# Kernel tuning notes

Hardware: AMD Instinct MI355X
Metric: run time of the kernel (lower is better)

The kernel has to match this reference:

```python
import jax, jax.numpy as jnp
import numpy as np

N, E, F, H, C, L = 50000, 800000, 32, 4, 32, 3
HC = H * C
NEG = 0.2  # leaky_relu negative slope (GATv2Conv default and explicit LeakyReLU(0.2))


def _gat_layer(x, src, dst, ea, Wl, bl, Wr, br, att, We, cb, lW, lb, bsc, bsh):
    # GATv2 linear transforms: [N, F] -> [N, H, C]
    xl = (x @ Wl + bl).reshape(N, H, C)
    xr = (x @ Wr + br).reshape(N, H, C)
    xj = xl[src]            # [E, H, C] messages from source nodes
    xi = xr[dst]            # [E, H, C] target-side features
    ep = (ea[:, None] @ We).reshape(E, H, C)  # edge-linear, edge_dim=1
    e = jax.nn.leaky_relu(xi + xj + ep, NEG)
    logits = jnp.einsum('ehc,hc->eh', e, att)            # [E, H]
    # segment softmax over destination node neighborhoods
    m = jax.ops.segment_max(logits, dst, num_segments=N)
    a = jnp.exp(logits - m[dst])
    denom = jax.ops.segment_sum(a, dst, num_segments=N)
    alpha = a / denom[dst]                               # [E, H]
    msg = xj * alpha[..., None]                          # [E, H, C]
    out = jax.ops.segment_sum(msg, dst, num_segments=N).reshape(N, HC) + cb
    # trailing per-layer MLP: Linear -> LeakyReLU(0.2) -> BatchNorm1d (eval, affine)
    h = jax.nn.leaky_relu(out @ lW + lb, NEG)
    return h * bsc + bsh


def setup_inputs() -> dict:
    key = jax.random.key(0)
    ks = jax.random.split(key, 24)
    s = 0.1
    inp = {
        'x': jax.random.normal(ks[0], (N, F), jnp.float32),
        'edge_index': jax.random.randint(ks[1], (2, E), 0, N, jnp.int32),
        'edge_attr': jax.random.normal(ks[2], (E,), jnp.float32),
        'batch': jnp.zeros((N,), jnp.int32),
        # stacked per-layer conv params (all 3 layers share shapes: F==hidden)
        'Wl': jax.random.normal(ks[3], (L, F, HC), jnp.float32) * s,
        'bl': jnp.zeros((L, HC), jnp.float32),
        'Wr': jax.random.normal(ks[4], (L, F, HC), jnp.float32) * s,
        'br': jnp.zeros((L, HC), jnp.float32),
        'att': jax.random.normal(ks[5], (L, H, C), jnp.float32) * s,
        'We': jax.random.normal(ks[6], (L, 1, HC), jnp.float32) * s,
        'conv_b': jnp.zeros((L, HC), jnp.float32),
        'lin_W': jax.random.normal(ks[7], (L, HC, F), jnp.float32) * s,
        'lin_b': jnp.zeros((L, F), jnp.float32),
        'bn_scale': jnp.ones((L, F), jnp.float32),
        'bn_shift': jnp.zeros((L, F), jnp.float32),
        # fcn head: hidden -> 256 -> 32 -> num_classes
        'W1': jax.random.normal(ks[8], (F, 256), jnp.float32) * s,
        'b1': jnp.zeros((256,), jnp.float32),
        'W2': jax.random.normal(ks[9], (256, 32), jnp.float32) * s,
        'b2': jnp.zeros((32,), jnp.float32),
        'W3': jax.random.normal(ks[10], (32, 2), jnp.float32) * s,
        'b3': jnp.zeros((2,), jnp.float32),
    }
    return inp


def reference(x, edge_index, edge_attr, batch, Wl, bl, Wr, br, att, We, conv_b,
              lin_W, lin_b, bn_scale, bn_shift, W1, b1, W2, b2, W3, b3):
    src, dst = edge_index[0], edge_index[1]
    ea = jnp.abs(edge_attr)
    h = x
    for i in range(L):
        h = _gat_layer(h, src, dst, ea, Wl[i], bl[i], Wr[i], br[i], att[i],
                       We[i], conv_b[i], lin_W[i], lin_b[i], bn_scale[i], bn_shift[i])
    # global mean pool over graphs in batch (single graph here, B=1)
    B = 1
    sums = jax.ops.segment_sum(h, batch, num_segments=B)
    cnts = jax.ops.segment_sum(jnp.ones((N, 1), h.dtype), batch, num_segments=B)
    g = sums / cnts
    g = jax.nn.leaky_relu(g @ W1 + b1, NEG)
    g = jax.nn.leaky_relu(g @ W2 + b2, NEG)
    return g @ W3 + b3
```

## Files before the change

kernel.cpp:

```cpp
#include <hip/hip_runtime.h>
#include <hip/hip_bf16.h>
#include <math.h>

#define NN 50000
#define EE 800000
#define HC 128
#define FF 32
#define NEG 0.2f


__global__ void k_hist(const int* __restrict__ dst, int* __restrict__ deg) {
    int e = blockIdx.x * 256 + threadIdx.x;
    if (e < EE) atomicAdd(&deg[dst[e]], 1);
}

__global__ void k_scan1(const int* __restrict__ deg, int* __restrict__ part) {
    __shared__ int sd[256];
    int b = blockIdx.x, t = threadIdx.x;
    int base = b * 1024 + t * 4;
    int s = 0;
#pragma unroll
    for (int i = 0; i < 4; ++i) { int idx = base + i; if (idx < NN) s += deg[idx]; }
    sd[t] = s; __syncthreads();
    for (int off = 128; off; off >>= 1) { if (t < off) sd[t] += sd[t + off]; __syncthreads(); }
    if (t == 0) part[b] = sd[0];
}

__global__ void k_scan2(int* __restrict__ part, int nb) {
    if (threadIdx.x == 0) {
        int run = 0;
        for (int i = 0; i < nb; ++i) { int v = part[i]; part[i] = run; run += v; }
    }
}

__global__ void k_scan3(const int* __restrict__ deg, const int* __restrict__ part,
                        int* __restrict__ rowptr) {
    __shared__ int sd[256];
    int b = blockIdx.x, t = threadIdx.x;
    int base = b * 1024 + t * 4;
    int v[4]; int mine = 0;
#pragma unroll
    for (int i = 0; i < 4; ++i) { int idx = base + i; v[i] = (idx < NN) ? deg[idx] : 0; mine += v[i]; }
    sd[t] = mine; __syncthreads();
    for (int off = 1; off < 256; off <<= 1) {
        int tmp = (t >= off) ? sd[t - off] : 0;
        __syncthreads();
        sd[t] += tmp;
        __syncthreads();
    }
    int run = sd[t] - mine + part[b];
#pragma unroll
    for (int i = 0; i < 4; ++i) { int idx = base + i; if (idx < NN) rowptr[idx] = run; run += v[i]; }
    if (b == 0 && t == 0) rowptr[NN] = EE;
}

__global__ void k_scatter(const int* __restrict__ src, const int* __restrict__ dst,
                          const float* __restrict__ ea, const int* __restrict__ rowptr,
                          int* __restrict__ fill, int2* __restrict__ pairs) {
    int e = blockIdx.x * 256 + threadIdx.x;
    if (e >= EE) return;
    int d = dst[e];
    int pos = rowptr[d] + atomicAdd(&fill[d], 1);
    pairs[pos] = make_int2(src[e], __float_as_int(fabsf(ea[e])));
}


__global__ __launch_bounds__(256) void k_dual_linear(
        const float* __restrict__ x,
        const float* __restrict__ Wl, const float* __restrict__ bl,
        const float* __restrict__ Wr, const float* __restrict__ br,
        float* __restrict__ xl, float* __restrict__ xr) {
    const int t = threadIdx.x;
    const int l = t & 63;
    const int half = l >> 5;
    const int lc = l & 31;
    const float* __restrict__ W  = half ? Wr : Wl;
    const float* __restrict__ bb = half ? br : bl;
    float* __restrict__ outp     = half ? xr : xl;

    float4 w[32];
#pragma unroll
    for (int k = 0; k < 32; ++k)
        w[k] = *(const float4*)(W + k * 128 + 4 * lc);
    const float4 bias = *(const float4*)(bb + 4 * lc);

    const int gw = blockIdx.x * 4 + (t >> 6);
    const int nW = gridDim.x * 4;
    const int q8 = 4 * (l & 7);

    int n = gw;
    if (n >= NN) return;
    float4 r0 = *(const float4*)(x + (size_t)n * 32 + q8);
    int n1 = n + nW < NN ? n + nW : n;
    float4 r1 = *(const float4*)(x + (size_t)n1 * 32 + q8);

    for (; n < NN; n += nW) {
        float4 cur = r0;
        r0 = r1;
        int np = n + 2 * nW < NN ? n + 2 * nW : n;
        r1 = *(const float4*)(x + (size_t)np * 32 + q8);

        float4 acc = bias;
#pragma unroll
        for (int q = 0; q < 8; ++q) {
            float vx = __shfl(cur.x, q, 8);
            float vy = __shfl(cur.y, q, 8);
            float vz = __shfl(cur.z, q, 8);
            float vw = __shfl(cur.w, q, 8);
            acc.x = fmaf(vx, w[4 * q + 0].x, acc.x);
            acc.y = fmaf(vx, w[4 * q + 0].y, acc.y);
            acc.z = fmaf(vx, w[4 * q + 0].z, acc.z);
            acc.w = fmaf(vx, w[4 * q + 0].w, acc.w);
            acc.x = fmaf(vy, w[4 * q + 1].x, acc.x);
            acc.y = fmaf(vy, w[4 * q + 1].y, acc.y);
            acc.z = fmaf(vy, w[4 * q + 1].z, acc.z);
            acc.w = fmaf(vy, w[4 * q + 1].w, acc.w);
            acc.x = fmaf(vz, w[4 * q + 2].x, acc.x);
            acc.y = fmaf(vz, w[4 * q + 2].y, acc.y);
            acc.z = fmaf(vz, w[4 * q + 2].z, acc.z);
            acc.w = fmaf(vz, w[4 * q + 2].w, acc.w);
            acc.x = fmaf(vw, w[4 * q + 3].x, acc.x);
            acc.y = fmaf(vw, w[4 * q + 3].y, acc.y);
            acc.z = fmaf(vw, w[4 * q + 3].z, acc.z);
            acc.w = fmaf(vw, w[4 * q + 3].w, acc.w);
        }
        *(float4*)(outp + (size_t)n * 128 + 4 * lc) = acc;
    }
}


__global__ __launch_bounds__(256) void k_gat_agg(
        const float* __restrict__ xl, const float* __restrict__ xr,
        const int* __restrict__ rowptr, const int2* __restrict__ pairs,
        const float* __restrict__ att,
        const float* __restrict__ Wev,
        const float* __restrict__ cb,
        float* __restrict__ outb) {
    const int l = threadIdx.x & 31;
    const int n = blockIdx.x * 8 + (threadIdx.x >> 5);
    const float4* __restrict__ xl4 = (const float4*)xl;

    float4 att4 = ((const float4*)att)[l];
    float4 we4  = ((const float4*)Wev)[l];
    float4 xr4  = ((const float4*)xr)[n * 32 + l];
    const int beg = rowptr[n], end = rowptr[n + 1];

    float m = -INFINITY, s = 0.f;
    float4 acc = make_float4(0.f, 0.f, 0.f, 0.f);

    int2 p0 = make_int2(0, 0), p1 = p0, p2 = p0, p3 = p0;
    float4 x0 = make_float4(0.f, 0.f, 0.f, 0.f), x1 = x0;
    if (beg     < end) p0 = pairs[beg];
    if (beg + 1 < end) p1 = pairs[beg + 1];
    if (beg + 2 < end) p2 = pairs[beg + 2];
    if (beg + 3 < end) p3 = pairs[beg + 3];
    if (beg     < end) x0 = xl4[(size_t)p0.x * 32 + l];
    if (beg + 1 < end) x1 = xl4[(size_t)p1.x * 32 + l];

#pragma unroll 2
    for (int j = beg; j < end; ++j) {
        int2 pn = p0; float4 xn = x0;
        if (j + 4 < end) pn = pairs[j + 4];
        if (j + 2 < end) xn = xl4[(size_t)p2.x * 32 + l];

        float sea = __int_as_float(p0.y);
        float4 v;
        v.x = fmaf(sea, we4.x, xr4.x + x0.x);
        v.y = fmaf(sea, we4.y, xr4.y + x0.y);
        v.z = fmaf(sea, we4.z, xr4.z + x0.z);
        v.w = fmaf(sea, we4.w, xr4.w + x0.w);
        v.x = fmaxf(v.x, NEG * v.x);
        v.y = fmaxf(v.y, NEG * v.y);
        v.z = fmaxf(v.z, NEG * v.z);
        v.w = fmaxf(v.w, NEG * v.w);
        float pl = v.x * att4.x;
        pl = fmaf(v.y, att4.y, pl);
        pl = fmaf(v.z, att4.z, pl);
        pl = fmaf(v.w, att4.w, pl);
        pl += __shfl_xor(pl, 4);
        pl += __shfl_xor(pl, 2);
        pl += __shfl_xor(pl, 1);

        if (pl <= m) {
            float e = __expf(pl - m);
            s += e;
            acc.x = fmaf(e, x0.x, acc.x);
            acc.y = fmaf(e, x0.y, acc.y);
            acc.z = fmaf(e, x0.z, acc.z);
            acc.w = fmaf(e, x0.w, acc.w);
        } else {
            float c = __expf(m - pl);
            s = fmaf(s, c, 1.f);
            acc.x = fmaf(acc.x, c, x0.x);
            acc.y = fmaf(acc.y, c, x0.y);
            acc.z = fmaf(acc.z, c, x0.z);
            acc.w = fmaf(acc.w, c, x0.w);
            m = pl;
        }
        p0 = p1; p1 = p2; p2 = p3; p3 = pn;
        x0 = x1; x1 = xn;
    }

    float inv = (s > 0.f) ? 1.f / s : 0.f;
    float4 cb4 = ((const float4*)cb)[l];
    float4 o;
    o.x = fmaf(acc.x, inv, cb4.x);
    o.y = fmaf(acc.y, inv, cb4.y);
    o.z = fmaf(acc.z, inv, cb4.z);
    o.w = fmaf(acc.w, inv, cb4.w);
    ((float4*)outb)[n * 32 + l] = o;
}


__global__ __launch_bounds__(256) void k_mlp_bn(
        const float* __restrict__ outb,
        const float* __restrict__ lW, const float* __restrict__ lb,
        const float* __restrict__ bsc, const float* __restrict__ bsh,
        float* __restrict__ h) {
    const int t = threadIdx.x;
    const int l = t & 63;
    const int half = l >> 5;
    const int cg = (l >> 2) & 7;
    const int kg = l & 3;

    float4 w[32];
#pragma unroll
    for (int kl = 0; kl < 32; ++kl)
        w[kl] = *(const float4*)(lW + (size_t)(32 * kg + kl) * 32 + 4 * cg);

    const float4 bias = (kg == 0) ? *(const float4*)(lb + 4 * cg)
                                  : make_float4(0.f, 0.f, 0.f, 0.f);
    const float4 sc4 = *(const float4*)(bsc + 4 * cg);
    const float4 sh4 = *(const float4*)(bsh + 4 * cg);

    const int gw = blockIdx.x * 4 + (t >> 6);
    const int nW = gridDim.x * 4;
    const int quad = 4 * (l & 31);
    const int kg8 = kg * 8;

    int p = gw;
    if (p >= NN / 2) return;
    float4 r0 = *(const float4*)(outb + (size_t)(2 * p + half) * 128 + quad);
    int p1i = p + nW < NN / 2 ? p + nW : p;
    float4 r1 = *(const float4*)(outb + (size_t)(2 * p1i + half) * 128 + quad);

    for (; p < NN / 2; p += nW) {
        float4 cur = r0;
        r0 = r1;
        int pp = p + 2 * nW < NN / 2 ? p + 2 * nW : p;
        r1 = *(const float4*)(outb + (size_t)(2 * pp + half) * 128 + quad);

        float4 acc = bias;
#pragma unroll
        for (int j = 0; j < 8; ++j) {
            float vx = __shfl(cur.x, kg8 + j, 32);
            float vy = __shfl(cur.y, kg8 + j, 32);
            float vz = __shfl(cur.z, kg8 + j, 32);
            float vw = __shfl(cur.w, kg8 + j, 32);
            acc.x = fmaf(vx, w[4 * j + 0].x, acc.x);
            acc.y = fmaf(vx, w[4 * j + 0].y, acc.y);
            acc.z = fmaf(vx, w[4 * j + 0].z, acc.z);
            acc.w = fmaf(vx, w[4 * j + 0].w, acc.w);
            acc.x = fmaf(vy, w[4 * j + 1].x, acc.x);
            acc.y = fmaf(vy, w[4 * j + 1].y, acc.y);
            acc.z = fmaf(vy, w[4 * j + 1].z, acc.z);
            acc.w = fmaf(vy, w[4 * j + 1].w, acc.w);
            acc.x = fmaf(vz, w[4 * j + 2].x, acc.x);
            acc.y = fmaf(vz, w[4 * j + 2].y, acc.y);
            acc.z = fmaf(vz, w[4 * j + 2].z, acc.z);
            acc.w = fmaf(vz, w[4 * j + 2].w, acc.w);
            acc.x = fmaf(vw, w[4 * j + 3].x, acc.x);
            acc.y = fmaf(vw, w[4 * j + 3].y, acc.y);
            acc.z = fmaf(vw, w[4 * j + 3].z, acc.z);
            acc.w = fmaf(vw, w[4 * j + 3].w, acc.w);
        }
        acc.x += __shfl_xor(acc.x, 1); acc.x += __shfl_xor(acc.x, 2);
        acc.y += __shfl_xor(acc.y, 1); acc.y += __shfl_xor(acc.y, 2);
        acc.z += __shfl_xor(acc.z, 1); acc.z += __shfl_xor(acc.z, 2);
        acc.w += __shfl_xor(acc.w, 1); acc.w += __shfl_xor(acc.w, 2);

        if (kg == 0) {
            float4 o;
            o.x = fmaxf(acc.x, NEG * acc.x);
            o.y = fmaxf(acc.y, NEG * acc.y);
            o.z = fmaxf(acc.z, NEG * acc.z);
            o.w = fmaxf(acc.w, NEG * acc.w);
            o.x = fmaf(o.x, sc4.x, sh4.x);
            o.y = fmaf(o.y, sc4.y, sh4.y);
            o.z = fmaf(o.z, sc4.z, sh4.z);
            o.w = fmaf(o.w, sc4.w, sh4.w);
            *(float4*)(h + (size_t)(2 * p + half) * 32 + 4 * cg) = o;
        }
    }
}


__global__ void k_colsum(const float* __restrict__ h, float* __restrict__ g) {
    __shared__ float sd[256];
    int t = threadIdx.x;
    int col = t & 31, r = t >> 5;
    float local = 0.f;
    for (int row = blockIdx.x * 8 + r; row < NN; row += gridDim.x * 8)
        local += h[row * FF + col];
    sd[t] = local; __syncthreads();
    if (r < 4) sd[t] += sd[t + 128];
    __syncthreads();
    if (r < 2) sd[t] += sd[t + 64];
    __syncthreads();
    if (r < 1) atomicAdd(&g[col], sd[t] + sd[t + 32]);
}


__global__ void k_head(const float* __restrict__ g,
                       const float* __restrict__ W1, const float* __restrict__ b1,
                       const float* __restrict__ W2, const float* __restrict__ b2,
                       const float* __restrict__ W3, const float* __restrict__ b3,
                       float* __restrict__ out) {
    __shared__ float gv[32];
    __shared__ float h1[256];
    __shared__ float h2[32];
    int t = threadIdx.x;
    if (t < 32) gv[t] = g[t] * (1.0f / NN);
    __syncthreads();
    float acc = b1[t];
#pragma unroll 8
    for (int k = 0; k < 32; ++k) acc += gv[k] * W1[k * 256 + t];
    h1[t] = acc > 0.f ? acc : NEG * acc;
    __syncthreads();
    if (t < 32) {
        float a = b2[t];
        for (int k = 0; k < 256; ++k) a += h1[k] * W2[k * 32 + t];
        h2[t] = a > 0.f ? a : NEG * a;
    }
    __syncthreads();
    if (t < 2) {
        float a = b3[t];
#pragma unroll
        for (int k = 0; k < 32; ++k) a += h2[k] * W3[k * 2 + t];
        out[t] = a;
    }
}


static inline size_t alignup(size_t x) { return (x + 255) & ~size_t(255); }

extern "C" void kernel_launch(void* const* d_in, const int* in_sizes, int n_in,
                              void* d_out, int out_size, void* d_ws, size_t ws_size,
                              hipStream_t stream) {
    const float* x     = (const float*)d_in[0];
    const int*   eidx  = (const int*)d_in[1];
    const float* eattr = (const float*)d_in[2];
    const float* Wl    = (const float*)d_in[4];
    const float* bl    = (const float*)d_in[5];
    const float* Wr    = (const float*)d_in[6];
    const float* br    = (const float*)d_in[7];
    const float* att   = (const float*)d_in[8];
    const float* We    = (const float*)d_in[9];
    const float* cb    = (const float*)d_in[10];
    const float* lW    = (const float*)d_in[11];
    const float* lb    = (const float*)d_in[12];
    const float* bsc   = (const float*)d_in[13];
    const float* bsh   = (const float*)d_in[14];
    const float* W1    = (const float*)d_in[15];
    const float* b1    = (const float*)d_in[16];
    const float* W2    = (const float*)d_in[17];
    const float* b2    = (const float*)d_in[18];
    const float* W3    = (const float*)d_in[19];
    const float* b3    = (const float*)d_in[20];

    const int* srcp = eidx;
    const int* dstp = eidx + EE;

    char* ws = (char*)d_ws;
    size_t off = 0;
    float* xl     = (float*)(ws + off); off += alignup((size_t)NN * HC * 4);
    float* xr     = (float*)(ws + off); off += alignup((size_t)NN * HC * 4);
    float* outb   = (float*)(ws + off); off += alignup((size_t)NN * HC * 4);
    float* hA     = (float*)(ws + off); off += alignup((size_t)NN * FF * 4);
    float* hB     = (float*)(ws + off); off += alignup((size_t)NN * FF * 4);
    int2*  pairs  = (int2*) (ws + off); off += alignup((size_t)EE * 8);
    int*   rowptr = (int*)  (ws + off); off += alignup((size_t)(NN + 1) * 4);
    int*   deg    = (int*)  (ws + off); off += alignup((size_t)NN * 4);
    int*   fill   = (int*)  (ws + off); off += alignup((size_t)NN * 4);
    int*   part   = (int*)  (ws + off); off += alignup(64 * 4);
    float* g      = (float*)(ws + off); off += alignup(32 * 4);

    hipMemsetAsync(deg, 0, (size_t)NN * 4, stream);
    hipMemsetAsync(fill, 0, (size_t)NN * 4, stream);
    hipMemsetAsync(g, 0, 32 * 4, stream);

    const int nChunk = (NN + 1023) / 1024;
    k_hist<<<(EE + 255) / 256, 256, 0, stream>>>(dstp, deg);
    k_scan1<<<nChunk, 256, 0, stream>>>(deg, part);
    k_scan2<<<1, 64, 0, stream>>>(part, nChunk);
    k_scan3<<<nChunk, 256, 0, stream>>>(deg, part, rowptr);
    k_scatter<<<(EE + 255) / 256, 256, 0, stream>>>(srcp, dstp, eattr, rowptr, fill, pairs);

    const float* cur = x;
    float* hbuf[2] = {hA, hB};
    for (int i = 0; i < 3; ++i) {
        k_dual_linear<<<768, 256, 0, stream>>>(cur, Wl + i * FF * HC, bl + i * HC,
                                               Wr + i * FF * HC, br + i * HC, xl, xr);
        k_gat_agg<<<NN / 8, 256, 0, stream>>>(xl, xr, rowptr, pairs,
                                              att + i * HC, We + i * HC, cb + i * HC, outb);
        k_mlp_bn<<<768, 256, 0, stream>>>(outb, lW + i * HC * FF, lb + i * FF,
                                          bsc + i * FF, bsh + i * FF, hbuf[i & 1]);
        cur = hbuf[i & 1];
    }

    k_colsum<<<128, 256, 0, stream>>>(cur, g);
    k_head<<<1, 256, 0, stream>>>(g, W1, b1, W2, b2, W3, b3, (float*)d_out);
}
```

Baseline: 555.2 us.

## Merge scan kernels, make online softmax branchless, drop memsets and colsum atomics

Replaces the three-kernel prefix scan with a single-block scan, which cuts launch count but serialises about 200 elements per thread in one block. The GAT aggregation loop becomes branchless: each edge computes two exps with a running max instead of a divergent branch. Prefetch indices are clamped rather than guarded, and addresses are computed with byte shifts. The colsum atomics are replaced by per-block partials that the head kernel reduces. The deg and fill memsets are merged into one and the g memset is dropped.

```diff
diff --git a/kernel.cpp b/kernel.cpp
--- a/kernel.cpp
+++ b/kernel.cpp
@@ -14,44 +14,28 @@
     if (e < EE) atomicAdd(&deg[dst[e]], 1);
 }
 
-__global__ void k_scan1(const int* __restrict__ deg, int* __restrict__ part) {
-    __shared__ int sd[256];
-    int b = blockIdx.x, t = threadIdx.x;
-    int base = b * 1024 + t * 4;
+__global__ __launch_bounds__(256) void k_scan(const int* __restrict__ deg,
+                                              int* __restrict__ rowptr) {
+    __shared__ int sums[256];
+    const int t = threadIdx.x;
+    const int CH = (NN + 255) >> 8;
+    const int b0 = t * CH;
+    const int b1 = b0 + CH < NN ? b0 + CH : NN;
     int s = 0;
-#pragma unroll
-    for (int i = 0; i < 4; ++i) { int idx = base + i; if (idx < NN) s += deg[idx]; }
-    sd[t] = s; __syncthreads();
-    for (int off = 128; off; off >>= 1) { if (t < off) sd[t] += sd[t + off]; __syncthreads(); }
-    if (t == 0) part[b] = sd[0];
-}
-
-__global__ void k_scan2(int* __restrict__ part, int nb) {
-    if (threadIdx.x == 0) {
-        int run = 0;
-        for (int i = 0; i < nb; ++i) { int v = part[i]; part[i] = run; run += v; }
-    }
-}
-
-__global__ void k_scan3(const int* __restrict__ deg, const int* __restrict__ part,
-                        int* __restrict__ rowptr) {
-    __shared__ int sd[256];
-    int b = blockIdx.x, t = threadIdx.x;
-    int base = b * 1024 + t * 4;
-    int v[4]; int mine = 0;
-#pragma unroll
-    for (int i = 0; i < 4; ++i) { int idx = base + i; v[i] = (idx < NN) ? deg[idx] : 0; mine += v[i]; }
-    sd[t] = mine; __syncthreads();
+    for (int i = b0; i < b1; ++i) s += deg[i];
+    sums[t] = s;
+    __syncthreads();
+    int acc = s;
     for (int off = 1; off < 256; off <<= 1) {
-        int tmp = (t >= off) ? sd[t - off] : 0;
+        int tmp = (t >= off) ? sums[t - off] : 0;
         __syncthreads();
-        sd[t] += tmp;
+        acc += tmp;
+        sums[t] = acc;
         __syncthreads();
     }
-    int run = sd[t] - mine + part[b];
-#pragma unroll
-    for (int i = 0; i < 4; ++i) { int idx = base + i; if (idx < NN) rowptr[idx] = run; run += v[i]; }
-    if (b == 0 && t == 0) rowptr[NN] = EE;
+    int run = acc - s;
+    for (int i = b0; i < b1; ++i) { rowptr[i] = run; run += deg[i]; }
+    if (t == 255) rowptr[NN] = EE;
 }
 
 __global__ void k_scatter(const int* __restrict__ src, const int* __restrict__ dst,
@@ -138,67 +122,61 @@
         float* __restrict__ outb) {
     const int l = threadIdx.x & 31;
     const int n = blockIdx.x * 8 + (threadIdx.x >> 5);
-    const float4* __restrict__ xl4 = (const float4*)xl;
+    const char* __restrict__ xlp = (const char*)xl + (l << 4);
 
     float4 att4 = ((const float4*)att)[l];
     float4 we4  = ((const float4*)Wev)[l];
     float4 xr4  = ((const float4*)xr)[n * 32 + l];
     const int beg = rowptr[n], end = rowptr[n + 1];
+    const int last = end - 1;
 
     float m = -INFINITY, s = 0.f;
     float4 acc = make_float4(0.f, 0.f, 0.f, 0.f);
 
-    int2 p0 = make_int2(0, 0), p1 = p0, p2 = p0, p3 = p0;
-    float4 x0 = make_float4(0.f, 0.f, 0.f, 0.f), x1 = x0;
-    if (beg     < end) p0 = pairs[beg];
-    if (beg + 1 < end) p1 = pairs[beg + 1];
-    if (beg + 2 < end) p2 = pairs[beg + 2];
-    if (beg + 3 < end) p3 = pairs[beg + 3];
-    if (beg     < end) x0 = xl4[(size_t)p0.x * 32 + l];
-    if (beg + 1 < end) x1 = xl4[(size_t)p1.x * 32 + l];
+    if (beg < end) {
+        int2 p0 = pairs[beg];
+        int2 p1 = pairs[beg + 1 < last ? beg + 1 : last];
+        int2 p2 = pairs[beg + 2 < last ? beg + 2 : last];
+        float4 x0 = *(const float4*)(xlp + (p0.x << 9));
+        float4 x1 = *(const float4*)(xlp + (p1.x << 9));
 
 #pragma unroll 2
-    for (int j = beg; j < end; ++j) {
-        int2 pn = p0; float4 xn = x0;
-        if (j + 4 < end) pn = pairs[j + 4];
-        if (j + 2 < end) xn = xl4[(size_t)p2.x * 32 + l];
-
-        float sea = __int_as_float(p0.y);
-        float4 v;
-        v.x = fmaf(sea, we4.x, xr4.x + x0.x);
-        v.y = fmaf(sea, we4.y, xr4.y + x0.y);
-        v.z = fmaf(sea, we4.z, xr4.z + x0.z);
-        v.w = fmaf(sea, we4.w, xr4.w + x0.w);
-        v.x = fmaxf(v.x, NEG * v.x);
-        v.y = fmaxf(v.y, NEG * v.y);
-        v.z = fmaxf(v.z, NEG * v.z);
-        v.w = fmaxf(v.w, NEG * v.w);
-        float pl = v.x * att4.x;
-        pl = fmaf(v.y, att4.y, pl);
-        pl = fmaf(v.z, att4.z, pl);
-        pl = fmaf(v.w, att4.w, pl);
-        pl += __shfl_xor(pl, 4);
-        pl += __shfl_xor(pl, 2);
-        pl += __shfl_xor(pl, 1);
-
-        if (pl <= m) {
-            float e = __expf(pl - m);
-            s += e;
-            acc.x = fmaf(e, x0.x, acc.x);
-            acc.y = fmaf(e, x0.y, acc.y);
-            acc.z = fmaf(e, x0.z, acc.z);
-            acc.w = fmaf(e, x0.w, acc.w);
-        } else {
-            float c = __expf(m - pl);
-            s = fmaf(s, c, 1.f);
-            acc.x = fmaf(acc.x, c, x0.x);
-            acc.y = fmaf(acc.y, c, x0.y);
-            acc.z = fmaf(acc.z, c, x0.z);
-            acc.w = fmaf(acc.w, c, x0.w);
-            m = pl;
+        for (int j = beg; j <= last; ++j) {
+            int jn = j + 3 < last ? j + 3 : last;
+            int2 pn = pairs[jn];
+            float4 xn = *(const float4*)(xlp + (p2.x << 9));
+
+            float sea = __int_as_float(p0.y);
+            float4 v;
+            v.x = fmaf(sea, we4.x, xr4.x + x0.x);
+            v.y = fmaf(sea, we4.y, xr4.y + x0.y);
+            v.z = fmaf(sea, we4.z, xr4.z + x0.z);
+            v.w = fmaf(sea, we4.w, xr4.w + x0.w);
+            v.x = fmaxf(v.x, NEG * v.x);
+            v.y = fmaxf(v.y, NEG * v.y);
+            v.z = fmaxf(v.z, NEG * v.z);
+            v.w = fmaxf(v.w, NEG * v.w);
+            float pl = v.x * att4.x;
+            pl = fmaf(v.y, att4.y, pl);
+            pl = fmaf(v.z, att4.z, pl);
+            pl = fmaf(v.w, att4.w, pl);
+            pl += __shfl_xor(pl, 4);
+            pl += __shfl_xor(pl, 2);
+            pl += __shfl_xor(pl, 1);
+
+            float mn = fmaxf(m, pl);
+            float c  = __expf(m - mn);
+            float e  = __expf(pl - mn);
+            s = fmaf(s, c, e);
+            acc.x = fmaf(acc.x, c, e * x0.x);
+            acc.y = fmaf(acc.y, c, e * x0.y);
+            acc.z = fmaf(acc.z, c, e * x0.z);
+            acc.w = fmaf(acc.w, c, e * x0.w);
+            m = mn;
+
+            p0 = p1; p1 = p2; p2 = pn;
+            x0 = x1; x1 = xn;
         }
-        p0 = p1; p1 = p2; p2 = p3; p3 = pn;
-        x0 = x1; x1 = xn;
     }
 
     float inv = (s > 0.f) ? 1.f / s : 0.f;
@@ -295,7 +273,7 @@
 }
 
 
-__global__ void k_colsum(const float* __restrict__ h, float* __restrict__ g) {
+__global__ void k_colsum(const float* __restrict__ h, float* __restrict__ part_g) {
     __shared__ float sd[256];
     int t = threadIdx.x;
     int col = t & 31, r = t >> 5;
@@ -307,20 +285,30 @@
     __syncthreads();
     if (r < 2) sd[t] += sd[t + 64];
     __syncthreads();
-    if (r < 1) atomicAdd(&g[col], sd[t] + sd[t + 32]);
-}
-
-
-__global__ void k_head(const float* __restrict__ g,
+    if (r < 1) part_g[blockIdx.x * 32 + col] = sd[t] + sd[t + 32];
+}
+
+
+__global__ void k_head(const float* __restrict__ part_g,
                        const float* __restrict__ W1, const float* __restrict__ b1,
                        const float* __restrict__ W2, const float* __restrict__ b2,
                        const float* __restrict__ W3, const float* __restrict__ b3,
                        float* __restrict__ out) {
+    __shared__ float red[256];
     __shared__ float gv[32];
     __shared__ float h1[256];
     __shared__ float h2[32];
     int t = threadIdx.x;
-    if (t < 32) gv[t] = g[t] * (1.0f / NN);
+    int col = t & 31, r = t >> 5;
+    float lsum = 0.f;
+#pragma unroll
+    for (int k = 0; k < 16; ++k) lsum += part_g[(r + 8 * k) * 32 + col];
+    red[t] = lsum; __syncthreads();
+    if (r < 4) red[t] += red[t + 128];
+    __syncthreads();
+    if (r < 2) red[t] += red[t + 64];
+    __syncthreads();
+    if (r < 1) gv[col] = (red[t] + red[t + 32]) * (1.0f / NN);
     __syncthreads();
     float acc = b1[t];
 #pragma unroll 8
@@ -382,18 +370,12 @@
     int*   rowptr = (int*)  (ws + off); off += alignup((size_t)(NN + 1) * 4);
     int*   deg    = (int*)  (ws + off); off += alignup((size_t)NN * 4);
     int*   fill   = (int*)  (ws + off); off += alignup((size_t)NN * 4);
-    int*   part   = (int*)  (ws + off); off += alignup(64 * 4);
-    float* g      = (float*)(ws + off); off += alignup(32 * 4);
-
-    hipMemsetAsync(deg, 0, (size_t)NN * 4, stream);
-    hipMemsetAsync(fill, 0, (size_t)NN * 4, stream);
-    hipMemsetAsync(g, 0, 32 * 4, stream);
-
-    const int nChunk = (NN + 1023) / 1024;
+    float* part_g = (float*)(ws + off); off += alignup(128 * 32 * 4);
+
+    hipMemsetAsync(deg, 0, alignup((size_t)NN * 4) + (size_t)NN * 4, stream);
+
     k_hist<<<(EE + 255) / 256, 256, 0, stream>>>(dstp, deg);
-    k_scan1<<<nChunk, 256, 0, stream>>>(deg, part);
-    k_scan2<<<1, 64, 0, stream>>>(part, nChunk);
-    k_scan3<<<nChunk, 256, 0, stream>>>(deg, part, rowptr);
+    k_scan<<<1, 256, 0, stream>>>(deg, rowptr);
     k_scatter<<<(EE + 255) / 256, 256, 0, stream>>>(srcp, dstp, eattr, rowptr, fill, pairs);
 
     const float* cur = x;
@@ -408,6 +390,6 @@
         cur = hbuf[i & 1];
     }
 
-    k_colsum<<<128, 256, 0, stream>>>(cur, g);
-    k_head<<<1, 256, 0, stream>>>(g, W1, b1, W2, b2, W3, b3, (float*)d_out);
-}
+    k_colsum<<<128, 256, 0, stream>>>(cur, part_g);
+    k_head<<<1, 256, 0, stream>>>(part_g, W1, b1, W2, b2, W3, b3, (float*)d_out);
+}
```

Result: slower. 632.3 us (+13.9%).
